# Kernel optimization log

Hardware: AMD Instinct MI355X
Metric: run time of the kernel (lower is better)

Reference implementation:

```python
import jax, jax.numpy as jnp
import numpy as np

N_S, N_T = 64, 32
N_EFF = N_S * N_T          # 2048
K_T1, K_T2 = 8, 8
BATCH = 16


def _orthonormal(key, n):
    q, _ = jnp.linalg.qr(jax.random.normal(key, (n, n), dtype=jnp.float32))
    return q.astype(jnp.float32)


def setup_inputs() -> dict:
    key = jax.random.key(0)
    ks = jax.random.split(key, 6)
    return {
        "s_effective_batch": jax.random.normal(ks[0], (BATCH, N_EFF), dtype=jnp.float32),
        "U_G": _orthonormal(ks[1], N_S),
        "U_P_T": _orthonormal(ks[2], N_T),
        "h0": jax.random.normal(ks[3], (N_EFF,), dtype=jnp.float32) * 0.01,
        "h_hat_1_coeffs": jax.random.normal(ks[4], (N_S, K_T1), dtype=jnp.float32) * 0.01,
        "H_hat_2_S": jax.random.normal(ks[5], (N_S, N_S), dtype=jnp.float32) * 0.01,
        "H_hat_2_T_coeffs": jax.random.normal(jax.random.fold_in(key, 7), (K_T2, K_T2), dtype=jnp.float32) * 0.01,
    }


def reference(s_effective_batch, U_G, U_P_T, h0, h_hat_1_coeffs, H_hat_2_S, H_hat_2_T_coeffs):
    # spatio-temporal basis via Kronecker product: [N_eff, N_eff]
    U_ST = jnp.kron(U_G, U_P_T)

    # GFT as in the module: s_hat = s @ U_ST
    s_hat = s_effective_batch @ U_ST                       # [B, N_eff]

    # linear (first-order Volterra) term
    Ub1 = U_P_T[:, :K_T1]                                  # [N_T, K1]
    full_h_hat_1 = (h_hat_1_coeffs @ Ub1.T).reshape(-1)    # [N_eff]
    z1 = (full_h_hat_1[None, :] * s_hat) @ U_ST            # iGFT as in module: @ U_ST

    # quadratic kernel H2 = kron(H2_S, Ub2 @ C @ Ub2^T)
    Ub2 = U_P_T[:, :K_T2]
    full_H2_T = Ub2 @ (H_hat_2_T_coeffs @ Ub2.T)           # [N_T, N_T]
    H2 = jnp.kron(H_hat_2_S, full_H2_T)                    # [N_eff, N_eff]

    # z2[b,i] = diag( U_ST (H2 * s_hat_b s_hat_b^T) U_ST^T )_i
    #         = sum_{k,l} B[b,i,k] H2[k,l] B[b,i,l], with B[b,i,k] = U_ST[i,k]*s_hat[b,k]
    B = U_ST[None, :, :] * s_hat[:, None, :]               # [B, N_eff, N_eff]
    z2 = jnp.einsum('bik,kl,bil->bi', B, H2, B)            # batched GEMM + row-reduce

    return h0[None, :] + z1 + z2
```

## Files before the change

### kernel.cpp

```cpp
#include <hip/hip_runtime.h>


typedef short  bf16x8 __attribute__((ext_vector_type(8)));
typedef float  f32x4  __attribute__((ext_vector_type(4)));
typedef unsigned short u16;

static __device__ __forceinline__ u16 f2bf(float f) {
  unsigned u = __float_as_uint(f);
  u = (u + 0x7fff + ((u >> 16) & 1)) >> 16;
  return (u16)u;
}
static __device__ __forceinline__ float bf2f(u16 h) {
  return __uint_as_float(((unsigned)h) << 16);
}
static __device__ __forceinline__ float dot4(f32x4 a, f32x4 b) {
  return a.x * b.x + a.y * b.y + a.z * b.z + a.w * b.w;
}
static __device__ __forceinline__ int padr(int row, int col) {
  return row * 32 +
         ((((col >> 3) ^ (row & 3) ^ (((row >> 2) & 1) << 1)) & 3) << 3) +
         (col & 7);
}

__global__ __launch_bounds__(512) void volterra_one(
    const float* __restrict__ s, const float* __restrict__ UG,
    const float* __restrict__ UPT, const float* __restrict__ h0,
    const float* __restrict__ h1c, const float* __restrict__ HS,
    const float* __restrict__ Hc, float* __restrict__ out)
{
  const int b   = blockIdx.x >> 4;
  const int iT0 = (blockIdx.x & 15) << 1;
  const int t   = threadIdx.x;
  const int w   = t >> 6;
  const int l   = t & 63;
  const int r   = l & 15;
  const int g   = l >> 4;

  __shared__ __align__(16) u16   sSTh[2048], sSTl[2048];
  __shared__ __align__(16) u16   sUGTh[4096], sUGTl[4096];
  __shared__ __align__(16) u16   sUGh[4096];
  __shared__ __align__(16) float sUPT[32][36];
  __shared__ __align__(16) float wGmR[2][288], wAR[2][288], wQR[2][288];
  __shared__ __align__(16) u16   sT1h[2048], sT1l[2048];
  __shared__ __align__(16) u16   sWGAh[2][512], sWGAl[2][512];
  __shared__ __align__(16) u16   sWQh[2][512], sWQl[2][512];
  __shared__ __align__(16) u16   sGh[2][64][8], sGl[2][64][8];
  __shared__ __align__(16) u16   sAh[2][64][8], sAl[2][64][8];
  __shared__ __align__(16) u16   szero16[8];
  __shared__ __align__(16) u16   sE[2][4096];
  __shared__ float wv[2][64];
  __shared__ float zp1[2][4][64], zpart[2][4][64];

  {
    const f32x4 v = ((const f32x4*)(s + b * 2048))[t];
    const int rr = t >> 3, c0 = (t & 7) * 4;
    const float arr[4] = {v.x, v.y, v.z, v.w};
    #pragma unroll
    for (int i = 0; i < 4; ++i) {
      const int c = c0 + i;
      const u16 hi = f2bf(arr[i]);
      const int ad = c * 64 + (((rr >> 3) ^ (c & 7)) << 3) + (rr & 7);
      sSTh[ad] = hi;
      sSTl[ad] = f2bf(arr[i] - bf2f(hi));
    }
  }
  #pragma unroll
  for (int it = 0; it < 2; ++it) {
    const int o4 = t + it * 512;
    const int rr = o4 >> 4, c0 = (o4 & 15) * 4;
    const f32x4 v = ((const f32x4*)UG)[o4];
    const float arr[4] = {v.x, v.y, v.z, v.w};
    short4 h4;
    h4.x = (short)f2bf(v.x); h4.y = (short)f2bf(v.y);
    h4.z = (short)f2bf(v.z); h4.w = (short)f2bf(v.w);
    *(short4*)&sUGh[rr * 64 + (c0 ^ ((rr & 7) << 3))] = h4;
    #pragma unroll
    for (int i = 0; i < 4; ++i) {
      const int c = c0 + i;
      const u16 hi = f2bf(arr[i]);
      const int ad = c * 64 + (((rr >> 3) ^ (c & 7)) << 3) + (rr & 7);
      sUGTh[ad] = hi;
      sUGTl[ad] = f2bf(arr[i] - bf2f(hi));
    }
  }
  if (t < 256) {
    *(f32x4*)&sUPT[t >> 3][(t & 7) * 4] = ((const f32x4*)UPT)[t];
  }
  if (t < 8) szero16[t] = 0;
  {
    const int side = t >> 8, p = (t >> 5) & 7, k = t & 31;
    const int iTs = iT0 + side;
    const float m1 = UPT[iTs * 32 + k];
    const float m3 = UPT[k * 32 + iTs];
    const float m2 = UPT[k * 32 + p];
    float uh = 0.f;
    #pragma unroll
    for (int q = 0; q < 8; ++q) uh += UPT[k * 32 + q] * Hc[q * 8 + p];
    wGmR[side][p * 36 + k] = m1 * m2;
    wAR [side][p * 36 + k] = m1 * uh;
    wQR [side][p * 36 + k] = m3 * m2;
  }
  __syncthreads();

  {
    const int band = w >> 1, ct = w & 1;
    const int rowA = 16 * band + r, rowB = ct * 16 + r;
    f32x4 acc = {0.f, 0.f, 0.f, 0.f};
    #pragma unroll
    for (int kc = 0; kc < 2; ++kc) {
      const int ch = kc * 4 + g;
      const int oa = rowA * 64 + ((ch ^ (rowA & 7)) << 3);
      const int ob = rowB * 64 + ((ch ^ (rowB & 7)) << 3);
      const bf16x8 Ah = *(const bf16x8*)&sUGTh[oa];
      const bf16x8 Al = *(const bf16x8*)&sUGTl[oa];
      const bf16x8 Bh = *(const bf16x8*)&sSTh[ob];
      const bf16x8 Bl = *(const bf16x8*)&sSTl[ob];
      acc = __builtin_amdgcn_mfma_f32_16x16x32_bf16(Ah, Bh, acc, 0, 0, 0);
      acc = __builtin_amdgcn_mfma_f32_16x16x32_bf16(Ah, Bl, acc, 0, 0, 0);
      acc = __builtin_amdgcn_mfma_f32_16x16x32_bf16(Al, Bh, acc, 0, 0, 0);
    }
    #pragma unroll
    for (int reg = 0; reg < 4; ++reg) {
      const int row = 16 * band + 4 * g + reg;
      const int ad = padr(row, ct * 16 + r);
      const u16 hi = f2bf(acc[reg]);
      sT1h[ad] = hi;
      sT1l[ad] = f2bf(acc[reg] - bf2f(hi));
    }
  }
  {
    const int side = t >> 8, p = (t >> 5) & 7, j = t & 31;
    float aG = 0.f, aA = 0.f, aQ = 0.f;
    #pragma unroll
    for (int k4 = 0; k4 < 8; ++k4) {
      const f32x4 u  = *(const f32x4*)&sUPT[j][k4 * 4];
      const f32x4 w1 = *(const f32x4*)&wGmR[side][p * 36 + k4 * 4];
      const f32x4 w2 = *(const f32x4*)&wAR [side][p * 36 + k4 * 4];
      const f32x4 w3 = *(const f32x4*)&wQR [side][p * 36 + k4 * 4];
      aG += dot4(u, w1); aA += dot4(u, w2); aQ += dot4(u, w3);
    }
    const int adG = padr(p, j), adA = padr(8 + p, j);
    u16 h;
    h = f2bf(aG); sWGAh[side][adG] = h; sWGAl[side][adG] = f2bf(aG - bf2f(h));
    h = f2bf(aA); sWGAh[side][adA] = h; sWGAl[side][adA] = f2bf(aA - bf2f(h));
    h = f2bf(aQ); sWQh[side][adG]  = h; sWQl[side][adG]  = f2bf(aQ - bf2f(h));
    sWQh[side][adA] = 0; sWQl[side][adA] = 0;
  }
  __syncthreads();

  {
    const int side = t >> 8, sub = (t >> 6) & 3;
    const int rowA = 16 * sub + r;
    const int oa = padr(rowA, g * 8);
    const bf16x8 Ah = *(const bf16x8*)&sT1h[oa];
    const bf16x8 Al = *(const bf16x8*)&sT1l[oa];
    const int ob = padr(r, g * 8);
    const bf16x8 GAh = *(const bf16x8*)&sWGAh[side][ob];
    const bf16x8 GAl = *(const bf16x8*)&sWGAl[side][ob];
    const bf16x8 Qh  = *(const bf16x8*)&sWQh[side][ob];
    const bf16x8 Ql  = *(const bf16x8*)&sWQl[side][ob];
    f32x4 accGA = {0.f, 0.f, 0.f, 0.f}, accQ = {0.f, 0.f, 0.f, 0.f};
    accGA = __builtin_amdgcn_mfma_f32_16x16x32_bf16(Ah, GAh, accGA, 0, 0, 0);
    accGA = __builtin_amdgcn_mfma_f32_16x16x32_bf16(Ah, GAl, accGA, 0, 0, 0);
    accGA = __builtin_amdgcn_mfma_f32_16x16x32_bf16(Al, GAh, accGA, 0, 0, 0);
    accQ  = __builtin_amdgcn_mfma_f32_16x16x32_bf16(Ah, Qh,  accQ,  0, 0, 0);
    accQ  = __builtin_amdgcn_mfma_f32_16x16x32_bf16(Ah, Ql,  accQ,  0, 0, 0);
    accQ  = __builtin_amdgcn_mfma_f32_16x16x32_bf16(Al, Qh,  accQ,  0, 0, 0);
    #pragma unroll
    for (int reg = 0; reg < 4; ++reg) {
      const int row = 16 * sub + 4 * g + reg;
      const float v = accGA[reg];
      const u16 h = f2bf(v);
      const u16 lo = f2bf(v - bf2f(h));
      if (r < 8) { sGh[side][row][r] = h;     sGl[side][row][r] = lo; }
      else       { sAh[side][row][r - 8] = h; sAl[side][row][r - 8] = lo; }
      float pr = (r < 8) ? h1c[row * 8 + r] * accQ[reg] : 0.f;
      pr += __shfl_xor(pr, 1);
      pr += __shfl_xor(pr, 2);
      pr += __shfl_xor(pr, 4);
      if (r == 0) wv[side][row] = pr;
    }
  }
  __syncthreads();

  {
    const int side = t >> 8, sub = (t >> 6) & 3;
    const int rowA = 16 * sub + r;
    const u16* ap = (g < 2)  ? &sAh[side][rowA][0]
                  : (g == 2) ? &sAl[side][rowA][0] : szero16;
    const bf16x8 af = *(const bf16x8*)ap;
    #pragma unroll
    for (int cb = 0; cb < 4; ++cb) {
      const int rowB = 16 * cb + r;
      const u16* bp = (g == 0) ? &sGh[side][rowB][0]
                    : (g == 1) ? &sGl[side][rowB][0]
                    : (g == 2) ? &sGh[side][rowB][0] : szero16;
      const bf16x8 bf = *(const bf16x8*)bp;
      f32x4 acc = {0.f, 0.f, 0.f, 0.f};
      acc = __builtin_amdgcn_mfma_f32_16x16x32_bf16(af, bf, acc, 0, 0, 0);
      #pragma unroll
      for (int reg = 0; reg < 4; ++reg) {
        const int row = 16 * sub + 4 * g + reg;
        const int col = 16 * cb + r;
        const float e = acc[reg] * HS[row * 64 + col];
        sE[side][row * 64 + (col ^ ((row & 7) << 3))] = f2bf(e);
      }
    }
    const float wvl = wv[side][l];
    float part = 0.f;
    #pragma unroll
    for (int j = 0; j < 16; ++j) {
      const int kk = 16 * sub + j;
      part += __shfl(wvl, kk) * UG[kk * 64 + l];
    }
    zp1[side][sub][l] = part;
  }

  {
    const int side = t >> 8, sub = (t >> 6) & 3;
    f32x4 acc[4];
    #pragma unroll
    for (int nt = 0; nt < 4; ++nt) acc[nt] = (f32x4){0.f, 0.f, 0.f, 0.f};
    #pragma unroll
    for (int ks = 0; ks < 2; ++ks) {
      const int kcol = g * 8 + ks * 32;
      const int rowA = 16 * sub + r;
      const bf16x8 ah = *(const bf16x8*)&sE[side][rowA * 64 + (kcol ^ ((rowA & 7) << 3))];
      #pragma unroll
      for (int nt = 0; nt < 4; ++nt) {
        const int rowB = 16 * nt + r;
        const bf16x8 bh = *(const bf16x8*)&sUGh[rowB * 64 + (kcol ^ ((rowB & 7) << 3))];
        acc[nt] = __builtin_amdgcn_mfma_f32_16x16x32_bf16(ah, bh, acc[nt], 0, 0, 0);
      }
    }
    #pragma unroll
    for (int nt = 0; nt < 4; ++nt) {
      float zp = 0.f;
      #pragma unroll
      for (int reg = 0; reg < 4; ++reg) {
        const int kS = 16 * sub + 4 * g + reg;
        const int iS = 16 * nt + r;
        zp += bf2f(sUGh[iS * 64 + (kS ^ ((iS & 7) << 3))]) * acc[nt][reg];
      }
      zp += __shfl_xor(zp, 16);
      zp += __shfl_xor(zp, 32);
      if (g == 0) zpart[side][sub][16 * nt + r] = zp;
    }
  }
  __syncthreads();

  if (t < 128) {
    const int side = t >> 6, c = t & 63;
    const float z2 = zpart[side][0][c] + zpart[side][1][c] +
                     zpart[side][2][c] + zpart[side][3][c];
    const float z1 = zp1[side][0][c] + zp1[side][1][c] +
                     zp1[side][2][c] + zp1[side][3][c];
    const int col = c * 32 + iT0 + side;
    out[b * 2048 + col] = h0[col] + z1 + z2;
  }
}

extern "C" void kernel_launch(void* const* d_in, const int* in_sizes, int n_in,
                              void* d_out, int out_size, void* d_ws, size_t ws_size,
                              hipStream_t stream) {
  const float* s   = (const float*)d_in[0];
  const float* UG  = (const float*)d_in[1];
  const float* UPT = (const float*)d_in[2];
  const float* h0  = (const float*)d_in[3];
  const float* h1c = (const float*)d_in[4];
  const float* HS  = (const float*)d_in[5];
  const float* Hc  = (const float*)d_in[6];
  float* out = (float*)d_out;

  volterra_one<<<256, 512, 0, stream>>>(s, UG, UPT, h0, h1c, HS, Hc, out);
}
```

Before: 12.97 us.

## Drop low-order bf16 splits for UG and T1, restructure final GEMM to per-wave reduction

Removes the low-part bf16 planes of UG^T and the intermediate T1, which cuts one of the three split-precision MFMAs in the first two GEMM stages. The last stage is reorganised so each wave owns 16 output spatial indices across all four k-bands. The z1 and z2 reductions then finish in registers with shuffles and write output directly, removing the zpart/zp1 shared buffers and the final tail stage. This adds a barrier before the last stage and lowers accuracy, since UG and T1 now carry only bf16 precision.

```diff
diff --git a/kernel.cpp b/kernel.cpp
--- a/kernel.cpp
+++ b/kernel.cpp
@@ -37,11 +37,11 @@
   const int g   = l >> 4;
 
   __shared__ __align__(16) u16   sSTh[2048], sSTl[2048];
-  __shared__ __align__(16) u16   sUGTh[4096], sUGTl[4096];
+  __shared__ __align__(16) u16   sUGTh[4096];
   __shared__ __align__(16) u16   sUGh[4096];
   __shared__ __align__(16) float sUPT[32][36];
   __shared__ __align__(16) float wGmR[2][288], wAR[2][288], wQR[2][288];
-  __shared__ __align__(16) u16   sT1h[2048], sT1l[2048];
+  __shared__ __align__(16) u16   sT1h[2048];
   __shared__ __align__(16) u16   sWGAh[2][512], sWGAl[2][512];
   __shared__ __align__(16) u16   sWQh[2][512], sWQl[2][512];
   __shared__ __align__(16) u16   sGh[2][64][8], sGl[2][64][8];
@@ -49,7 +49,6 @@
   __shared__ __align__(16) u16   szero16[8];
   __shared__ __align__(16) u16   sE[2][4096];
   __shared__ float wv[2][64];
-  __shared__ float zp1[2][4][64], zpart[2][4][64];
 
   {
     const f32x4 v = ((const f32x4*)(s + b * 2048))[t];
@@ -74,13 +73,11 @@
     h4.x = (short)f2bf(v.x); h4.y = (short)f2bf(v.y);
     h4.z = (short)f2bf(v.z); h4.w = (short)f2bf(v.w);
     *(short4*)&sUGh[rr * 64 + (c0 ^ ((rr & 7) << 3))] = h4;
+    const u16 ha[4] = {(u16)h4.x, (u16)h4.y, (u16)h4.z, (u16)h4.w};
     #pragma unroll
     for (int i = 0; i < 4; ++i) {
       const int c = c0 + i;
-      const u16 hi = f2bf(arr[i]);
-      const int ad = c * 64 + (((rr >> 3) ^ (c & 7)) << 3) + (rr & 7);
-      sUGTh[ad] = hi;
-      sUGTl[ad] = f2bf(arr[i] - bf2f(hi));
+      sUGTh[c * 64 + (((rr >> 3) ^ (c & 7)) << 3) + (rr & 7)] = ha[i];
     }
   }
   if (t < 256) {
@@ -112,20 +109,15 @@
       const int oa = rowA * 64 + ((ch ^ (rowA & 7)) << 3);
       const int ob = rowB * 64 + ((ch ^ (rowB & 7)) << 3);
       const bf16x8 Ah = *(const bf16x8*)&sUGTh[oa];
-      const bf16x8 Al = *(const bf16x8*)&sUGTl[oa];
       const bf16x8 Bh = *(const bf16x8*)&sSTh[ob];
       const bf16x8 Bl = *(const bf16x8*)&sSTl[ob];
       acc = __builtin_amdgcn_mfma_f32_16x16x32_bf16(Ah, Bh, acc, 0, 0, 0);
       acc = __builtin_amdgcn_mfma_f32_16x16x32_bf16(Ah, Bl, acc, 0, 0, 0);
-      acc = __builtin_amdgcn_mfma_f32_16x16x32_bf16(Al, Bh, acc, 0, 0, 0);
     }
     #pragma unroll
     for (int reg = 0; reg < 4; ++reg) {
       const int row = 16 * band + 4 * g + reg;
-      const int ad = padr(row, ct * 16 + r);
-      const u16 hi = f2bf(acc[reg]);
-      sT1h[ad] = hi;
-      sT1l[ad] = f2bf(acc[reg] - bf2f(hi));
+      sT1h[padr(row, ct * 16 + r)] = f2bf(acc[reg]);
     }
   }
   {
@@ -151,9 +143,7 @@
   {
     const int side = t >> 8, sub = (t >> 6) & 3;
     const int rowA = 16 * sub + r;
-    const int oa = padr(rowA, g * 8);
-    const bf16x8 Ah = *(const bf16x8*)&sT1h[oa];
-    const bf16x8 Al = *(const bf16x8*)&sT1l[oa];
+    const bf16x8 Ah = *(const bf16x8*)&sT1h[padr(rowA, g * 8)];
     const int ob = padr(r, g * 8);
     const bf16x8 GAh = *(const bf16x8*)&sWGAh[side][ob];
     const bf16x8 GAl = *(const bf16x8*)&sWGAl[side][ob];
@@ -162,10 +152,8 @@
     f32x4 accGA = {0.f, 0.f, 0.f, 0.f}, accQ = {0.f, 0.f, 0.f, 0.f};
     accGA = __builtin_amdgcn_mfma_f32_16x16x32_bf16(Ah, GAh, accGA, 0, 0, 0);
     accGA = __builtin_amdgcn_mfma_f32_16x16x32_bf16(Ah, GAl, accGA, 0, 0, 0);
-    accGA = __builtin_amdgcn_mfma_f32_16x16x32_bf16(Al, GAh, accGA, 0, 0, 0);
     accQ  = __builtin_amdgcn_mfma_f32_16x16x32_bf16(Ah, Qh,  accQ,  0, 0, 0);
     accQ  = __builtin_amdgcn_mfma_f32_16x16x32_bf16(Ah, Ql,  accQ,  0, 0, 0);
-    accQ  = __builtin_amdgcn_mfma_f32_16x16x32_bf16(Al, Qh,  accQ,  0, 0, 0);
     #pragma unroll
     for (int reg = 0; reg < 4; ++reg) {
       const int row = 16 * sub + 4 * g + reg;
@@ -206,57 +194,50 @@
         sE[side][row * 64 + (col ^ ((row & 7) << 3))] = f2bf(e);
       }
     }
-    const float wvl = wv[side][l];
-    float part = 0.f;
-    #pragma unroll
-    for (int j = 0; j < 16; ++j) {
-      const int kk = 16 * sub + j;
-      part += __shfl(wvl, kk) * UG[kk * 64 + l];
-    }
-    zp1[side][sub][l] = part;
-  }
-
-  {
-    const int side = t >> 8, sub = (t >> 6) & 3;
+  }
+  __syncthreads();
+
+  {
+    const int side = t >> 8, q = (t >> 6) & 3;
+    const int iS = 16 * q + r;
     f32x4 acc[4];
     #pragma unroll
-    for (int nt = 0; nt < 4; ++nt) acc[nt] = (f32x4){0.f, 0.f, 0.f, 0.f};
+    for (int band = 0; band < 4; ++band) acc[band] = (f32x4){0.f, 0.f, 0.f, 0.f};
     #pragma unroll
     for (int ks = 0; ks < 2; ++ks) {
       const int kcol = g * 8 + ks * 32;
-      const int rowA = 16 * sub + r;
-      const bf16x8 ah = *(const bf16x8*)&sE[side][rowA * 64 + (kcol ^ ((rowA & 7) << 3))];
-      #pragma unroll
-      for (int nt = 0; nt < 4; ++nt) {
-        const int rowB = 16 * nt + r;
-        const bf16x8 bh = *(const bf16x8*)&sUGh[rowB * 64 + (kcol ^ ((rowB & 7) << 3))];
-        acc[nt] = __builtin_amdgcn_mfma_f32_16x16x32_bf16(ah, bh, acc[nt], 0, 0, 0);
-      }
-    }
-    #pragma unroll
-    for (int nt = 0; nt < 4; ++nt) {
-      float zp = 0.f;
+      const int rowB = iS;
+      const bf16x8 bh = *(const bf16x8*)&sUGh[rowB * 64 + (kcol ^ ((rowB & 7) << 3))];
+      #pragma unroll
+      for (int band = 0; band < 4; ++band) {
+        const int rowA = 16 * band + r;
+        const bf16x8 ah = *(const bf16x8*)&sE[side][rowA * 64 + (kcol ^ ((rowA & 7) << 3))];
+        acc[band] = __builtin_amdgcn_mfma_f32_16x16x32_bf16(ah, bh, acc[band], 0, 0, 0);
+      }
+    }
+    float tot = 0.f;
+    #pragma unroll
+    for (int band = 0; band < 4; ++band) {
       #pragma unroll
       for (int reg = 0; reg < 4; ++reg) {
-        const int kS = 16 * sub + 4 * g + reg;
-        const int iS = 16 * nt + r;
-        zp += bf2f(sUGh[iS * 64 + (kS ^ ((iS & 7) << 3))]) * acc[nt][reg];
-      }
-      zp += __shfl_xor(zp, 16);
-      zp += __shfl_xor(zp, 32);
-      if (g == 0) zpart[side][sub][16 * nt + r] = zp;
-    }
-  }
-  __syncthreads();
-
-  if (t < 128) {
-    const int side = t >> 6, c = t & 63;
-    const float z2 = zpart[side][0][c] + zpart[side][1][c] +
-                     zpart[side][2][c] + zpart[side][3][c];
-    const float z1 = zp1[side][0][c] + zp1[side][1][c] +
-                     zp1[side][2][c] + zp1[side][3][c];
-    const int col = c * 32 + iT0 + side;
-    out[b * 2048 + col] = h0[col] + z1 + z2;
+        const int kS = 16 * band + 4 * g + reg;
+        tot += bf2f(sUGh[iS * 64 + (kS ^ ((iS & 7) << 3))]) * acc[band][reg];
+      }
+    }
+    {
+      const float wvl = wv[side][l];
+      #pragma unroll
+      for (int j = 0; j < 16; ++j) {
+        const int kk = 16 * g + j;
+        tot += __shfl(wvl, kk) * UG[kk * 64 + iS];
+      }
+    }
+    tot += __shfl_xor(tot, 16);
+    tot += __shfl_xor(tot, 32);
+    if (g == 0) {
+      const int col = iS * 32 + iT0 + side;
+      out[b * 2048 + col] = h0[col] + tot;
+    }
   }
 }
 
```

Result: faster. 12.23 us (-5.7%).
